# Performance work log

Hardware: AMD Instinct MI355X
Metric: run time of the kernel (lower is better)

## Reference

```python
import jax, jax.numpy as jnp
import numpy as np

B, D, M = 512, 1024, 32768
K, MULTI_K, AUX_K = 32, 128, 64
DEAD_THRESH = 256
MATRYOSHKA_SIZES = [4096, 16384, 32768]


def setup_inputs() -> dict:
    key = jax.random.key(0)
    k0, k1, k2, k3, k4, k5 = jax.random.split(key, 6)
    return {
        "x": jax.random.normal(k0, (B, D), dtype=jnp.float32),
        "W_enc": jax.random.normal(k1, (M, D), dtype=jnp.float32) * 0.02,
        "W_dec": jax.random.normal(k2, (D, M), dtype=jnp.float32) * 0.02,
        "input_bias": jax.random.normal(k3, (D,), dtype=jnp.float32) * 0.01,
        "neuron_bias": jax.random.normal(k4, (M,), dtype=jnp.float32) * 0.01,
        "steps_since_activation": jax.random.randint(k5, (M,), 0, 512, dtype=jnp.int64),
    }


def reference(x, W_enc, W_dec, input_bias, neuron_bias, steps_since_activation):
    xc = x - input_bias                                   # [B, D]
    pre_act = xc @ W_enc.T + neuron_bias                  # [B, M]

    topk_values, topk_indices = jax.lax.top_k(pre_act, K)
    topk_values = jax.nn.relu(topk_values)
    multik_values, multik_indices = jax.lax.top_k(pre_act, MULTI_K)
    multik_values = jax.nn.relu(multik_values)

    rows = jnp.arange(pre_act.shape[0])[:, None]
    activations = jnp.zeros_like(pre_act).at[rows, topk_indices].set(topk_values)
    multik_activations = jnp.zeros_like(pre_act).at[rows, multik_indices].set(multik_values)

    reconstruction = activations @ W_dec.T + input_bias
    multik_reconstruction = multik_activations @ W_dec.T + input_bias

    # matryoshka partial reconstructions (all sizes except the last/full one)
    neuron_ids = jnp.arange(M)
    matryoshka_recons = []
    for m_i in MATRYOSHKA_SIZES[:-1]:
        partial_acts = activations * (neuron_ids < m_i).astype(activations.dtype)
        matryoshka_recons.append(partial_acts @ W_dec.T + input_bias)

    # aux-k over dead neurons (steps incremented by 1 before the mask in torch)
    dead_mask = ((steps_since_activation + 1) > DEAD_THRESH).astype(pre_act.dtype)
    aux_values, aux_indices = jax.lax.top_k(pre_act * dead_mask, AUX_K)
    aux_values = jax.nn.relu(aux_values)

    return (reconstruction, multik_reconstruction,
            matryoshka_recons[0], matryoshka_recons[1],
            topk_indices, topk_values, aux_indices, aux_values)
```

## Files before the change

### kernel.cpp

```cpp
#include <hip/hip_runtime.h>
#include <stdint.h>

#define B_ 512
#define D_ 1024
#define M_ 32768

typedef _Float16 half8 __attribute__((ext_vector_type(8)));
typedef _Float16 half4 __attribute__((ext_vector_type(4)));
typedef float f32x4 __attribute__((ext_vector_type(4)));

__device__ __forceinline__ unsigned f2k(float f) {
    unsigned b = __float_as_uint(f);
    return (b & 0x80000000u) ? ~b : (b | 0x80000000u);
}
__device__ __forceinline__ float k2f(unsigned k) {
    unsigned b = (k & 0x80000000u) ? (k & 0x7FFFFFFFu) : ~k;
    return __uint_as_float(b);
}
__device__ __forceinline__ unsigned long long d2k(double d) {
    unsigned long long b = (unsigned long long)__double_as_longlong(d);
    return (b & 0x8000000000000000ull) ? ~b : (b | 0x8000000000000000ull);
}

__device__ __forceinline__ void gld16(const void* g, void* l) {
    __builtin_amdgcn_global_load_lds(
        (__attribute__((address_space(1))) void*)(uintptr_t)g,
        (__attribute__((address_space(3))) void*)(unsigned)(uintptr_t)l,
        16, 0, 0);
}

__global__ __launch_bounds__(256) void split_x_k(
    const float* __restrict__ x, const float* __restrict__ ib,
    _Float16* __restrict__ xh)
{
    int i = blockIdx.x * 256 + threadIdx.x;
    float4 v = ((const float4*)x)[i];
    float4 bb = ((const float4*)ib)[i & 255];
    float a0 = (v.x - bb.x) * 2048.0f;
    float a1 = (v.y - bb.y) * 2048.0f;
    float a2 = (v.z - bb.z) * 2048.0f;
    float a3 = (v.w - bb.w) * 2048.0f;
    half4 hv = {(_Float16)a0, (_Float16)a1, (_Float16)a2, (_Float16)a3};
    ((half4*)xh)[i] = hv;
}

__global__ __launch_bounds__(256, 4) void enc_tr(
    const _Float16* __restrict__ xhf,
    const float* __restrict__ wenc, const float* __restrict__ nb,
    float* __restrict__ preact,
    const float* __restrict__ wdec, float* __restrict__ wdt)
{
    __shared__ alignas(16) _Float16 lA[2][128 * 32];
    __shared__ alignas(16) _Float16 lB[2][2][64 * 32];
    __shared__ float ttile[32][33];

    const int tid = threadIdx.x;
    const int chunk = blockIdx.x >> 8;
    const int sub = (chunk >> 1) * 256 + (blockIdx.x & 255);

    if (chunk & 1) {
        const int tx = tid & 31, ty = tid >> 5;
        for (int s = 0; s < 16; ++s) {
            int tix = sub * 16 + s;
            int x0 = (tix & 1023) * 32;
            int y0 = (tix >> 10) * 32;
#pragma unroll
            for (int j = 0; j < 32; j += 8)
                ttile[ty + j][tx] = wdec[(size_t)(y0 + ty + j) * M_ + x0 + tx];
            __syncthreads();
#pragma unroll
            for (int j = 0; j < 32; j += 8)
                wdt[(size_t)(x0 + ty + j) * D_ + y0 + tx] = ttile[tx][ty + j];
            __syncthreads();
        }
        return;
    }

    const int lane = tid & 63;
    const int wv = tid >> 6;
    const int wvr = wv >> 1;
    const int wvc = wv & 1;

    const int bid = sub;
    const int lb = bid >> 3;
    const int j0 = ((bid & 7) * 64 + (lb >> 2)) * 64;
    const int i0 = (lb & 3) * 128;

    const int ln15 = lane & 15;
    const int kq = (lane >> 4) * 8;

    f32x4 acc1[4][2], acc2[4][2];
#pragma unroll
    for (int r = 0; r < 4; ++r)
#pragma unroll
        for (int c = 0; c < 2; ++c) {
            acc1[r][c] = (f32x4){0.f, 0.f, 0.f, 0.f};
            acc2[r][c] = (f32x4){0.f, 0.f, 0.f, 0.f};
        }

    const int o0 = tid * 16;
    const int o1 = o0 + 4096;
    const int rA0 = o0 >> 6, rA1 = o1 >> 6;
    const int cA0s = (o0 & 63) ^ (((rA0 >> 1) & 3) << 4);
    const int cA1s = (o1 & 63) ^ (((rA1 >> 1) & 3) << 4);

    const int rW = tid >> 2;
    const int c8 = (tid & 3) * 8;
    const int c8s = c8 ^ (((rW >> 1) & 3) << 3);

    const int rowA = wvr * 64 + ln15;
    const int rowB = wvc * 32 + ln15;

#define STAGEA(k0, s)                                                                      \
    do {                                                                                   \
        gld16((const char*)(xhf + (size_t)(i0 + rA0) * 1024 + (k0)) + cA0s, (char*)lA[s] + o0); \
        gld16((const char*)(xhf + (size_t)(i0 + rA1) * 1024 + (k0)) + cA1s, (char*)lA[s] + o1); \
    } while (0)

#define LOADB(k0)                                                                          \
    do {                                                                                   \
        const float* wp = wenc + (size_t)(j0 + rW) * 1024 + (k0) + c8;                     \
        wv0 = *(const float4*)wp;                                                          \
        wv1 = *(const float4*)(wp + 4);                                                    \
    } while (0)

#define CVT1(idx, f)                                                                       \
    do { float a_ = (f) * 2048.0f; _Float16 h_ = (_Float16)a_;                             \
         bh[idx] = h_; br[idx] = (_Float16)((a_ - (float)h_) * 2048.0f); } while (0)

#define WRITEB(s)                                                                          \
    do {                                                                                   \
        half8 bh, br;                                                                      \
        CVT1(0, wv0.x); CVT1(1, wv0.y); CVT1(2, wv0.z); CVT1(3, wv0.w);                    \
        CVT1(4, wv1.x); CVT1(5, wv1.y); CVT1(6, wv1.z); CVT1(7, wv1.w);                    \
        *(half8*)&lB[s][0][rW * 32 + c8s] = bh;                                            \
        *(half8*)&lB[s][1][rW * 32 + c8s] = br;                                            \
    } while (0)

    float4 wv0, wv1;
    LOADB(0);
    asm volatile("s_waitcnt vmcnt(0)" ::: "memory");
    WRITEB(0);
    STAGEA(0, 0);
    LOADB(32);
    STAGEA(32, 1);
    asm volatile("s_waitcnt vmcnt(2)" ::: "memory");
    WRITEB(1);
    asm volatile("s_waitcnt lgkmcnt(0)" ::: "memory");
    __builtin_amdgcn_s_barrier();

    int cur = 0;
    for (int k0 = 0; k0 < 1024; k0 += 32) {
        if (k0 + 64 < 1024) LOADB(k0 + 64);

        half8 aH[4], bH[2], bR[2];
#pragma unroll
        for (int r = 0; r < 4; ++r) {
            const int ra = rowA + r * 16;
            const int ka = kq ^ (((ra >> 1) & 3) << 3);
            aH[r] = *(const half8*)&lA[cur][ra * 32 + ka];
        }
#pragma unroll
        for (int c = 0; c < 2; ++c) {
            const int rb = rowB + c * 16;
            const int kb = kq ^ (((rb >> 1) & 3) << 3);
            bH[c] = *(const half8*)&lB[cur][0][rb * 32 + kb];
            bR[c] = *(const half8*)&lB[cur][1][rb * 32 + kb];
        }
#pragma unroll
        for (int r = 0; r < 4; ++r)
#pragma unroll
            for (int c = 0; c < 2; ++c) {
                acc1[r][c] = __builtin_amdgcn_mfma_f32_16x16x32_f16(aH[r], bH[c], acc1[r][c], 0, 0, 0);
                acc2[r][c] = __builtin_amdgcn_mfma_f32_16x16x32_f16(aH[r], bR[c], acc2[r][c], 0, 0, 0);
            }

        if (k0 + 32 < 1024) {
            asm volatile("s_waitcnt lgkmcnt(0)" ::: "memory");
            __builtin_amdgcn_s_barrier();

            if (k0 + 64 < 1024) {
                STAGEA(k0 + 64, cur);
                asm volatile("s_waitcnt vmcnt(2)" ::: "memory");
                WRITEB(cur);
            } else {
                asm volatile("s_waitcnt vmcnt(0)" ::: "memory");
            }
            asm volatile("s_waitcnt lgkmcnt(0)" ::: "memory");
            __builtin_amdgcn_s_barrier();
        }
        cur ^= 1;
    }
#undef STAGEA
#undef LOADB
#undef CVT1
#undef WRITEB

    const float s1 = 0x1p-22f, s2 = 0x1p-33f;
#pragma unroll
    for (int c = 0; c < 2; ++c) {
        int n = j0 + wvc * 32 + c * 16 + ln15;
        float nbv = nb[n];
#pragma unroll
        for (int r = 0; r < 4; ++r) {
            int mb = i0 + wvr * 64 + r * 16 + (lane >> 4) * 4;
#pragma unroll
            for (int e = 0; e < 4; ++e)
                preact[(size_t)(mb + e) * M_ + n] = acc1[r][c][e] * s1 + acc2[r][c][e] * s2 + nbv;
        }
    }
}

__global__ __launch_bounds__(1024, 4) void select_both(
    const float* __restrict__ preact, const int* __restrict__ steps,
    int* __restrict__ sel_idx, float* __restrict__ sel_val,
    int* __restrict__ auxcand)
{
    __shared__ unsigned histU[4096];
    __shared__ unsigned histM[4096];
    __shared__ unsigned coarseU[256];
    __shared__ unsigned coarseM[256];
    __shared__ unsigned long long candU[512];
    __shared__ unsigned long long candM[512];
    __shared__ unsigned cntU, cntM, thrU, thrM, cbU, cbM, cumU, cumM;

    const int t = threadIdx.x;
    const int b = blockIdx.x;
    const float* row = preact + (size_t)b * M_;

    for (int i = t; i < 4096; i += 1024) { histU[i] = 0; histM[i] = 0; }
    if (t < 512) { candU[t] = 0ULL; candM[t] = 0ULL; }
    if (t == 0) { cntU = 0; cntM = 0; }
    __syncthreads();

    unsigned deadmask = 0;
#pragma unroll
    for (int p = 0; p < 8; ++p) {
        int i = t + p * 1024;
        int4 sv = ((const int4*)steps)[i];
        unsigned mbits = 0;
        if (sv.x + 1 > 256) mbits |= 1u;
        if (sv.y + 1 > 256) mbits |= 2u;
        if (sv.z + 1 > 256) mbits |= 4u;
        if (sv.w + 1 > 256) mbits |= 8u;
        deadmask |= mbits << (p * 4);
    }

    float4 v[8];
#pragma unroll
    for (int p = 0; p < 8; ++p) {
        int i = t + p * 1024;
        v[p] = ((const float4*)row)[i];
        unsigned k0 = f2k(v[p].x) >> 20;
        unsigned k1 = f2k(v[p].y) >> 20;
        unsigned k2 = f2k(v[p].z) >> 20;
        unsigned k3 = f2k(v[p].w) >> 20;
        atomicAdd(&histU[k0], 1u);
        atomicAdd(&histU[k1], 1u);
        atomicAdd(&histU[k2], 1u);
        atomicAdd(&histU[k3], 1u);
        unsigned dm = deadmask >> (p * 4);
        if (dm & 1u) atomicAdd(&histM[k0], 1u);
        if (dm & 2u) atomicAdd(&histM[k1], 1u);
        if (dm & 4u) atomicAdd(&histM[k2], 1u);
        if (dm & 8u) atomicAdd(&histM[k3], 1u);
    }
    __syncthreads();

    if (t < 256) {
        unsigned s = 0;
#pragma unroll
        for (int j = 0; j < 16; ++j) s += histU[t * 16 + j];
        coarseU[t] = s;
    } else if (t < 512) {
        int c = t - 256;
        unsigned s = 0;
#pragma unroll
        for (int j = 0; j < 16; ++j) s += histM[c * 16 + j];
        coarseM[c] = s;
    }
    __syncthreads();

    for (int off = 1; off < 256; off <<= 1) {
        unsigned xv = 0;
        if (t < 256)      xv = coarseU[t] + (t + off < 256 ? coarseU[t + off] : 0u);
        else if (t < 512) { int c = t - 256; xv = coarseM[c] + (c + off < 256 ? coarseM[c + off] : 0u); }
        __syncthreads();
        if (t < 256)      coarseU[t] = xv;
        else if (t < 512) coarseM[t - 256] = xv;
        __syncthreads();
    }

    if (t < 256) {
        unsigned S = coarseU[t];
        unsigned Sn = (t < 255) ? coarseU[t + 1] : 0u;
        if (S >= 128u && (t == 255 || Sn < 128u)) { cbU = (unsigned)t; cumU = Sn; }
    } else if (t < 512) {
        int c = t - 256;
        unsigned S = coarseM[c];
        unsigned Sn = (c < 255) ? coarseM[c + 1] : 0u;
        if (S >= 64u && (c == 255 || Sn < 64u)) { cbM = (unsigned)c; cumM = Sn; }
        if (c == 0 && S < 64u) { cbM = 0u; cumM = Sn; }
    }
    __syncthreads();

    if (t == 0) {
        unsigned cum = cumU;
        int base = (int)cbU * 16, tb = base;
        for (int f = base + 15; f >= base; --f) {
            unsigned h = histU[f];
            if (cum + h >= 128u) { tb = f; break; }
            cum += h;
        }
        thrU = (unsigned)tb;
    }
    if (t == 64) {
        unsigned cum = cumM;
        int base = (int)cbM * 16, tb = base;
        for (int f = base + 15; f >= base; --f) {
            unsigned h = histM[f];
            if (cum + h >= 64u) { tb = f; break; }
            cum += h;
        }
        thrM = (unsigned)(tb > 0 ? tb - 1 : 0);
    }
    __syncthreads();

    const unsigned TU = thrU, TM = thrM;

#pragma unroll
    for (int p = 0; p < 8; ++p) {
        int i = t + p * 1024;
#pragma unroll
        for (int e = 0; e < 4; ++e) {
            float val = (e == 0) ? v[p].x : (e == 1) ? v[p].y : (e == 2) ? v[p].z : v[p].w;
            unsigned key = f2k(val);
            int m = i * 4 + e;
            if ((key >> 20) >= TU) {
                unsigned pz = atomicAdd(&cntU, 1u);
                if (pz < 512u) candU[pz] = ((unsigned long long)key << 32) | (unsigned)(~m);
            }
            if (((deadmask >> (p * 4 + e)) & 1u) && (key >> 20) >= TM) {
                unsigned pz = atomicAdd(&cntM, 1u);
                if (pz < 512u) candM[pz] = ((unsigned long long)key << 32) | (unsigned)(~m);
            }
        }
    }
    __syncthreads();

    {
        unsigned long long* arr = (t < 512) ? candU : candM;
        const unsigned i = (unsigned)t & 511u;
        for (unsigned kk = 2; kk <= 512; kk <<= 1) {
            for (unsigned j = kk >> 1; j > 0; j >>= 1) {
                unsigned ixj = i ^ j;
                if (ixj > i) {
                    bool desc = ((i & kk) == 0);
                    unsigned long long a = arr[i], c = arr[ixj];
                    if (desc ? (a < c) : (a > c)) { arr[i] = c; arr[ixj] = a; }
                }
                unsigned nj = (j > 1) ? (j >> 1) : ((kk << 1) <= 512u ? kk : 0u);
                if (j >= 64 || nj >= 64) __syncthreads();
                else asm volatile("s_waitcnt lgkmcnt(0)" ::: "memory");
            }
        }
    }
    __syncthreads();

    if (t < 128) {
        unsigned long long c = candU[t];
        unsigned m = ~(unsigned)c;
        float vv = k2f((unsigned)(c >> 32));
        sel_idx[b * 128 + t] = (int)m;
        sel_val[b * 128 + t] = vv > 0.f ? vv : 0.f;
    }
    if (t < 96) {
        unsigned long long c = candM[t];
        auxcand[b * 96 + t] = c ? (int)(~(unsigned)c) : -1;
    }
}

__global__ __launch_bounds__(256) void resdec_k(
    const float* __restrict__ x, const float* __restrict__ ib,
    const float* __restrict__ wenc, const float* __restrict__ nb,
    const int* __restrict__ sel_idx, const float* __restrict__ sel_val,
    const int* __restrict__ auxcand, const float* __restrict__ wdt,
    float* __restrict__ out_tidx, float* __restrict__ out_tval,
    float* __restrict__ out_aidx, float* __restrict__ out_aval,
    float* __restrict__ o_recon, float* __restrict__ o_multik,
    float* __restrict__ o_mat0, float* __restrict__ o_mat1)
{
    __shared__ double xcs[1024];
    __shared__ unsigned long long kU[64];
    __shared__ unsigned long long kM[128];
    __shared__ float vU[64];
    __shared__ float vM[128];
    __shared__ int sidx[128];
    __shared__ float sval[128];
    __shared__ int ridx[32];
    __shared__ float rval[32];

    const int b = blockIdx.x, t = threadIdx.x;
    for (int d = t; d < 1024; d += 256)
        xcs[d] = (double)x[(size_t)b * 1024 + d] - (double)ib[d];
    if (t < 128) { sidx[t] = sel_idx[b * 128 + t]; sval[t] = sel_val[b * 128 + t]; }
    if (t < 64)  { kU[t] = 0ULL; vU[t] = 0.f; }
    if (t < 128) { kM[t] = 0ULL; vM[t] = 0.f; }
    __syncthreads();

    int m = -1;
    if (t < 64) m = sidx[t];
    else if (t >= 64 && t < 160) m = auxcand[b * 96 + (t - 64)];
    if (m >= 0) {
        const float* w = wenc + (size_t)m * 1024;
        double a0 = 0.0, a1 = 0.0, a2 = 0.0, a3 = 0.0;
        for (int d = 0; d < 1024; d += 4) {
            float4 wv = *(const float4*)(w + d);
            a0 = fma((double)wv.x, xcs[d + 0], a0);
            a1 = fma((double)wv.y, xcs[d + 1], a1);
            a2 = fma((double)wv.z, xcs[d + 2], a2);
            a3 = fma((double)wv.w, xcs[d + 3], a3);
        }
        double v = ((a0 + a1) + (a2 + a3)) + (double)nb[m];
        unsigned long long key = (d2k(v) & 0xFFFFFFFFFFFF0000ull)
                               | (unsigned long long)((~(unsigned)m) & 0xFFFFu);
        float vf = (float)v;
        if (t < 64) { kU[t] = key; vU[t] = vf; }
        else        { kM[t - 64] = key; vM[t - 64] = vf; }
    }
    __syncthreads();

    for (unsigned kk = 2; kk <= 128; kk <<= 1) {
        for (unsigned j = kk >> 1; j > 0; j >>= 1) {
            unsigned i = (unsigned)t, ixj = i ^ j;
            if (kk <= 64 && i < 64 && ixj > i) {
                bool desc = ((i & kk) == 0);
                unsigned long long a = kU[i], c = kU[ixj];
                if (desc ? (a < c) : (a > c)) {
                    kU[i] = c; kU[ixj] = a;
                    float fa = vU[i]; vU[i] = vU[ixj]; vU[ixj] = fa;
                }
            }
            if (i < 128 && ixj > i) {
                bool desc = ((i & kk) == 0);
                unsigned long long a = kM[i], c = kM[ixj];
                if (desc ? (a < c) : (a > c)) {
                    kM[i] = c; kM[ixj] = a;
                    float fa = vM[i]; vM[i] = vM[ixj]; vM[ixj] = fa;
                }
            }
            __syncthreads();
        }
    }

    if (t < 32) {
        unsigned mm = (~(unsigned)kU[t]) & 0xFFFFu;
        float v = vU[t];
        float rv = v > 0.f ? v : 0.f;
        ridx[t] = (int)mm;
        rval[t] = rv;
        out_tidx[b * 32 + t] = (float)mm;
        out_tval[b * 32 + t] = rv;
    }
    if (t < 64) {
        unsigned mm = (~(unsigned)kM[t]) & 0xFFFFu;
        float v = vM[t];
        out_aidx[b * 64 + t] = (float)mm;
        out_aval[b * 64 + t] = v > 0.f ? v : 0.f;
    }
    __syncthreads();

    const int d = t * 4;
    float4 bias = *(const float4*)(ib + d);
    float4 mul = bias, rec = bias, m0 = bias, m1 = bias;

    for (int k = 0; k < 128; ++k) {
        float v = sval[k];
        float4 w = *(const float4*)(wdt + (size_t)sidx[k] * D_ + d);
        mul.x += v * w.x; mul.y += v * w.y; mul.z += v * w.z; mul.w += v * w.w;
    }
    for (int k = 0; k < 32; ++k) {
        int idx = ridx[k];
        float v = rval[k];
        float4 w = *(const float4*)(wdt + (size_t)idx * D_ + d);
        rec.x += v * w.x; rec.y += v * w.y; rec.z += v * w.z; rec.w += v * w.w;
        if (idx < 16384) {
            m1.x += v * w.x; m1.y += v * w.y; m1.z += v * w.z; m1.w += v * w.w;
            if (idx < 4096) {
                m0.x += v * w.x; m0.y += v * w.y; m0.z += v * w.z; m0.w += v * w.w;
            }
        }
    }
    size_t o = (size_t)b * D_ + d;
    *(float4*)(o_recon + o)  = rec;
    *(float4*)(o_multik + o) = mul;
    *(float4*)(o_mat0 + o)   = m0;
    *(float4*)(o_mat1 + o)   = m1;
}

extern "C" void kernel_launch(void* const* d_in, const int* in_sizes, int n_in,
                              void* d_out, int out_size, void* d_ws, size_t ws_size,
                              hipStream_t stream)
{
    const float* x     = (const float*)d_in[0];
    const float* wenc  = (const float*)d_in[1];
    const float* wdec  = (const float*)d_in[2];
    const float* ib    = (const float*)d_in[3];
    const float* nb    = (const float*)d_in[4];
    const int*   steps = (const int*)d_in[5];
    float* out = (float*)d_out;

    char* ws = (char*)d_ws;
    float*     preact  = (float*)ws;
    float*     wdt     = (float*)(ws + 67108864);
    _Float16*  xhf     = (_Float16*)(ws + 201326592);
    int*       auxcand = (int*)(ws + 201326592 + 2097152);
    int*       sel_idx = (int*)(ws + 206569472);
    float*     sel_val = (float*)(ws + 206831616);

    float* out_recon  = out;
    float* out_multik = out + 524288;
    float* out_mat0   = out + 1048576;
    float* out_mat1   = out + 1572864;
    float* out_tidx   = out + 2097152;
    float* out_tval   = out + 2097152 + 16384;
    float* out_aidx   = out + 2097152 + 32768;
    float* out_aval   = out + 2097152 + 32768 + 32768;

    split_x_k<<<dim3(512), dim3(256), 0, stream>>>(x, ib, xhf);
    enc_tr<<<dim3(4096), dim3(256), 0, stream>>>(xhf, wenc, nb, preact, wdec, wdt);
    select_both<<<dim3(512), dim3(1024), 0, stream>>>(preact, steps, sel_idx, sel_val, auxcand);
    resdec_k<<<dim3(512), dim3(256), 0, stream>>>(
        x, ib, wenc, nb, sel_idx, sel_val, auxcand, wdt,
        out_tidx, out_tval, out_aidx, out_aval,
        out_recon, out_multik, out_mat0, out_mat1);
}
```

Measured before the change: 548.3 us.

## Fuse selection and exact rescoring/decode into one per-row kernel

Merges the top-k selection kernel and the rescoring/decoder kernel into a single 1024-thread block per row, so candidate indices and values stay in shared memory and never round-trip through global memory. It also removes one kernel launch. The float64 rescoring dot product is now split across 4 threads per candidate (640 threads) with a shared partial-sum reduction, where before one thread handled each candidate. The decode now uses one output column per thread with scalar loads instead of float4. The cost is higher shared memory and register pressure, with occupancy hints lowered to 2 blocks, plus narrower memory accesses in the decode.

Result: no change. 541.2 us (-1.3%).

```diff
diff --git a/kernel.cpp b/kernel.cpp
--- a/kernel.cpp
+++ b/kernel.cpp
@@ -211,10 +211,15 @@
     }
 }
 
-__global__ __launch_bounds__(1024, 4) void select_both(
+__global__ __launch_bounds__(1024, 2) void selresdec(
     const float* __restrict__ preact, const int* __restrict__ steps,
-    int* __restrict__ sel_idx, float* __restrict__ sel_val,
-    int* __restrict__ auxcand)
+    const float* __restrict__ x, const float* __restrict__ ib,
+    const float* __restrict__ wenc, const float* __restrict__ nb,
+    const float* __restrict__ wdt,
+    float* __restrict__ out_tidx, float* __restrict__ out_tval,
+    float* __restrict__ out_aidx, float* __restrict__ out_aval,
+    float* __restrict__ o_recon, float* __restrict__ o_multik,
+    float* __restrict__ o_mat0, float* __restrict__ o_mat1)
 {
     __shared__ unsigned histU[4096];
     __shared__ unsigned histM[4096];
@@ -222,6 +227,17 @@
     __shared__ unsigned coarseM[256];
     __shared__ unsigned long long candU[512];
     __shared__ unsigned long long candM[512];
+    __shared__ double xcs[1024];
+    __shared__ double part[160][4];
+    __shared__ unsigned long long kU[64];
+    __shared__ unsigned long long kM[128];
+    __shared__ float vU[64];
+    __shared__ float vM[128];
+    __shared__ int sidx[128];
+    __shared__ float sval[128];
+    __shared__ int auxm[96];
+    __shared__ int ridx[32];
+    __shared__ float rval[32];
     __shared__ unsigned cntU, cntM, thrU, thrM, cbU, cbM, cumU, cumM;
 
     const int t = threadIdx.x;
@@ -231,6 +247,9 @@
     for (int i = t; i < 4096; i += 1024) { histU[i] = 0; histM[i] = 0; }
     if (t < 512) { candU[t] = 0ULL; candM[t] = 0ULL; }
     if (t == 0) { cntU = 0; cntM = 0; }
+    xcs[t] = (double)x[(size_t)b * 1024 + t] - (double)ib[t];
+    if (t < 64)  { kU[t] = 0ULL; vU[t] = 0.f; }
+    if (t < 128) { kM[t] = 0ULL; vM[t] = 0.f; }
     __syncthreads();
 
     unsigned deadmask = 0;
@@ -371,62 +390,44 @@
         unsigned long long c = candU[t];
         unsigned m = ~(unsigned)c;
         float vv = k2f((unsigned)(c >> 32));
-        sel_idx[b * 128 + t] = (int)m;
-        sel_val[b * 128 + t] = vv > 0.f ? vv : 0.f;
+        sidx[t] = (int)m;
+        sval[t] = vv > 0.f ? vv : 0.f;
     }
     if (t < 96) {
         unsigned long long c = candM[t];
-        auxcand[b * 96 + t] = c ? (int)(~(unsigned)c) : -1;
-    }
-}
-
-__global__ __launch_bounds__(256) void resdec_k(
-    const float* __restrict__ x, const float* __restrict__ ib,
-    const float* __restrict__ wenc, const float* __restrict__ nb,
-    const int* __restrict__ sel_idx, const float* __restrict__ sel_val,
-    const int* __restrict__ auxcand, const float* __restrict__ wdt,
-    float* __restrict__ out_tidx, float* __restrict__ out_tval,
-    float* __restrict__ out_aidx, float* __restrict__ out_aval,
-    float* __restrict__ o_recon, float* __restrict__ o_multik,
-    float* __restrict__ o_mat0, float* __restrict__ o_mat1)
-{
-    __shared__ double xcs[1024];
-    __shared__ unsigned long long kU[64];
-    __shared__ unsigned long long kM[128];
-    __shared__ float vU[64];
-    __shared__ float vM[128];
-    __shared__ int sidx[128];
-    __shared__ float sval[128];
-    __shared__ int ridx[32];
-    __shared__ float rval[32];
-
-    const int b = blockIdx.x, t = threadIdx.x;
-    for (int d = t; d < 1024; d += 256)
-        xcs[d] = (double)x[(size_t)b * 1024 + d] - (double)ib[d];
-    if (t < 128) { sidx[t] = sel_idx[b * 128 + t]; sval[t] = sel_val[b * 128 + t]; }
-    if (t < 64)  { kU[t] = 0ULL; vU[t] = 0.f; }
-    if (t < 128) { kM[t] = 0ULL; vM[t] = 0.f; }
-    __syncthreads();
-
-    int m = -1;
-    if (t < 64) m = sidx[t];
-    else if (t >= 64 && t < 160) m = auxcand[b * 96 + (t - 64)];
-    if (m >= 0) {
-        const float* w = wenc + (size_t)m * 1024;
-        double a0 = 0.0, a1 = 0.0, a2 = 0.0, a3 = 0.0;
-        for (int d = 0; d < 1024; d += 4) {
-            float4 wv = *(const float4*)(w + d);
-            a0 = fma((double)wv.x, xcs[d + 0], a0);
-            a1 = fma((double)wv.y, xcs[d + 1], a1);
-            a2 = fma((double)wv.z, xcs[d + 2], a2);
-            a3 = fma((double)wv.w, xcs[d + 3], a3);
-        }
-        double v = ((a0 + a1) + (a2 + a3)) + (double)nb[m];
-        unsigned long long key = (d2k(v) & 0xFFFFFFFFFFFF0000ull)
-                               | (unsigned long long)((~(unsigned)m) & 0xFFFFu);
-        float vf = (float)v;
-        if (t < 64) { kU[t] = key; vU[t] = vf; }
-        else        { kM[t - 64] = key; vM[t - 64] = vf; }
+        auxm[t] = c ? (int)(~(unsigned)c) : -1;
+    }
+    __syncthreads();
+
+    if (t < 640) {
+        const int ci = t >> 2, q = t & 3;
+        int m = (ci < 64) ? sidx[ci] : auxm[ci - 64];
+        if (m >= 0) {
+            const float* w = wenc + (size_t)m * 1024 + q * 256;
+            const double* xq = xcs + q * 256;
+            double a0 = 0.0, a1 = 0.0, a2 = 0.0, a3 = 0.0;
+            for (int d = 0; d < 256; d += 4) {
+                float4 wv = *(const float4*)(w + d);
+                a0 = fma((double)wv.x, xq[d + 0], a0);
+                a1 = fma((double)wv.y, xq[d + 1], a1);
+                a2 = fma((double)wv.z, xq[d + 2], a2);
+                a3 = fma((double)wv.w, xq[d + 3], a3);
+            }
+            part[ci][q] = ((a0 + a1) + (a2 + a3));
+        }
+    }
+    __syncthreads();
+
+    if (t < 160) {
+        int m = (t < 64) ? sidx[t] : auxm[t - 64];
+        if (m >= 0) {
+            double vd = ((part[t][0] + part[t][1]) + (part[t][2] + part[t][3])) + (double)nb[m];
+            unsigned long long key = (d2k(vd) & 0xFFFFFFFFFFFF0000ull)
+                                   | (unsigned long long)((~(unsigned)m) & 0xFFFFu);
+            float vf = (float)vd;
+            if (t < 64) { kU[t] = key; vU[t] = vf; }
+            else        { kM[t - 64] = key; vM[t - 64] = vf; }
+        }
     }
     __syncthreads();
 
@@ -455,8 +456,8 @@
 
     if (t < 32) {
         unsigned mm = (~(unsigned)kU[t]) & 0xFFFFu;
-        float v = vU[t];
-        float rv = v > 0.f ? v : 0.f;
+        float vv = vU[t];
+        float rv = vv > 0.f ? vv : 0.f;
         ridx[t] = (int)mm;
         rval[t] = rv;
         out_tidx[b * 32 + t] = (float)mm;
@@ -464,38 +465,37 @@
     }
     if (t < 64) {
         unsigned mm = (~(unsigned)kM[t]) & 0xFFFFu;
-        float v = vM[t];
+        float vv = vM[t];
         out_aidx[b * 64 + t] = (float)mm;
-        out_aval[b * 64 + t] = v > 0.f ? v : 0.f;
-    }
-    __syncthreads();
-
-    const int d = t * 4;
-    float4 bias = *(const float4*)(ib + d);
-    float4 mul = bias, rec = bias, m0 = bias, m1 = bias;
-
-    for (int k = 0; k < 128; ++k) {
-        float v = sval[k];
-        float4 w = *(const float4*)(wdt + (size_t)sidx[k] * D_ + d);
-        mul.x += v * w.x; mul.y += v * w.y; mul.z += v * w.z; mul.w += v * w.w;
-    }
-    for (int k = 0; k < 32; ++k) {
-        int idx = ridx[k];
-        float v = rval[k];
-        float4 w = *(const float4*)(wdt + (size_t)idx * D_ + d);
-        rec.x += v * w.x; rec.y += v * w.y; rec.z += v * w.z; rec.w += v * w.w;
-        if (idx < 16384) {
-            m1.x += v * w.x; m1.y += v * w.y; m1.z += v * w.z; m1.w += v * w.w;
-            if (idx < 4096) {
-                m0.x += v * w.x; m0.y += v * w.y; m0.z += v * w.z; m0.w += v * w.w;
-            }
-        }
-    }
-    size_t o = (size_t)b * D_ + d;
-    *(float4*)(o_recon + o)  = rec;
-    *(float4*)(o_multik + o) = mul;
-    *(float4*)(o_mat0 + o)   = m0;
-    *(float4*)(o_mat1 + o)   = m1;
+        out_aval[b * 64 + t] = vv > 0.f ? vv : 0.f;
+    }
+    __syncthreads();
+
+    {
+        const int d = t;
+        float bias = ib[d];
+        float mul = bias, rec = bias, m0 = bias, m1 = bias;
+        for (int k = 0; k < 128; ++k) {
+            float vv = sval[k];
+            float w = wdt[(size_t)sidx[k] * D_ + d];
+            mul += vv * w;
+        }
+        for (int k = 0; k < 32; ++k) {
+            int idx = ridx[k];
+            float vv = rval[k];
+            float w = wdt[(size_t)idx * D_ + d];
+            rec += vv * w;
+            if (idx < 16384) {
+                m1 += vv * w;
+                if (idx < 4096) m0 += vv * w;
+            }
+        }
+        size_t o = (size_t)b * D_ + d;
+        o_recon[o]  = rec;
+        o_multik[o] = mul;
+        o_mat0[o]   = m0;
+        o_mat1[o]   = m1;
+    }
 }
 
 extern "C" void kernel_launch(void* const* d_in, const int* in_sizes, int n_in,
@@ -514,9 +514,6 @@
     float*     preact  = (float*)ws;
     float*     wdt     = (float*)(ws + 67108864);
     _Float16*  xhf     = (_Float16*)(ws + 201326592);
-    int*       auxcand = (int*)(ws + 201326592 + 2097152);
-    int*       sel_idx = (int*)(ws + 206569472);
-    float*     sel_val = (float*)(ws + 206831616);
 
     float* out_recon  = out;
     float* out_multik = out + 524288;
@@ -529,9 +526,8 @@
 
     split_x_k<<<dim3(512), dim3(256), 0, stream>>>(x, ib, xhf);
     enc_tr<<<dim3(4096), dim3(256), 0, stream>>>(xhf, wenc, nb, preact, wdec, wdt);
-    select_both<<<dim3(512), dim3(1024), 0, stream>>>(preact, steps, sel_idx, sel_val, auxcand);
-    resdec_k<<<dim3(512), dim3(256), 0, stream>>>(
-        x, ib, wenc, nb, sel_idx, sel_val, auxcand, wdt,
+    selresdec<<<dim3(512), dim3(1024), 0, stream>>>(
+        preact, steps, x, ib, wenc, nb, wdt,
         out_tidx, out_tval, out_aidx, out_aval,
         out_recon, out_multik, out_mat0, out_mat1);
 }
```
